# Kernel tuning notes

Measured on AMD Instinct MI355X. Metric: run time of the kernel, lower is better.

## Reference

```python
import jax, jax.numpy as jnp
import numpy as np

STRIDES = (8, 16, 32)
INPUT = (640, 640)
NC = 80           # num_classes
CONF = 0.65       # conf_thr
IOU_THR = 0.65    # nms iou_threshold
K = 1000          # fixed candidate cap for jit-compatible NMS (padded/masked)


def _priors():
    # MlvlPointGenerator(offset=0, with_stride=True): per level, points at
    # (x*stride, y*stride) flattened y-major, format [cx, cy, stride, stride].
    ps = []
    for s in STRIDES:
        H, W = INPUT[0] // s, INPUT[1] // s
        yy, xx = jnp.meshgrid(jnp.arange(H, dtype=jnp.float32),
                              jnp.arange(W, dtype=jnp.float32), indexing='ij')
        cx = (xx * s).ravel()
        cy = (yy * s).ravel()
        st = jnp.full_like(cx, float(s))
        ps.append(jnp.stack([cx, cy, st, st], axis=-1))
    return jnp.concatenate(ps, axis=0)  # [8400, 4]


def _flatten(xs, c):
    # permute(0,2,3,1).reshape(B, -1, c) per level, concat over priors
    return jnp.concatenate(
        [x.transpose(0, 2, 3, 1).reshape(x.shape[0], -1, c) for x in xs], axis=1)


def _decode(priors, bp):
    # bp: [B, N, 4]; priors: [N, 4] (cx, cy, sw, sh)
    xys = bp[..., :2] * priors[:, 2:] + priors[:, :2]
    whs = jnp.exp(bp[..., 2:]) * priors[:, 2:]
    tl = xys - whs * 0.5
    br = xys + whs * 0.5
    return jnp.concatenate([tl, br], axis=-1)  # [B, N, 4] tlbr


def _iou(a, b):
    tl = jnp.maximum(a[:, None, :2], b[None, :, :2])
    br = jnp.minimum(a[:, None, 2:], b[None, :, 2:])
    wh = jnp.clip(br - tl, 0.0)
    inter = wh[..., 0] * wh[..., 1]
    area = lambda x: (x[:, 2] - x[:, 0]) * (x[:, 3] - x[:, 1])
    union = area(a)[:, None] + area(b)[None, :] - inter
    return inter / (union + 1e-6)


def _nms_single(cls_s, obj_s, boxes):
    # cls_s: [N, NC] sigmoid scores; obj_s: [N]; boxes: [N, 4]
    max_s = cls_s.max(axis=-1)
    labels = jnp.argmax(cls_s, axis=-1)
    score = max_s * obj_s
    valid = score >= CONF                       # confidence mask
    sc = jnp.where(valid, score, 0.0)
    top_sc, idx = jax.lax.top_k(sc, K)          # sorted descending -> greedy order
    b = boxes[idx]
    lab = labels[idx]
    v = valid[idx]
    # class-aware (batched) NMS: offset boxes per label so classes never overlap
    max_coord = jnp.max(jnp.abs(b)) + 1.0
    ob = b + (lab.astype(b.dtype) * max_coord)[:, None]
    iou = _iou(ob, ob)                          # [K, K]
    j = jnp.arange(K)
    def body(i, keep):
        sup = (iou[i] > IOU_THR) & (j > i)
        return jnp.where(keep[i] & v[i], keep & (~sup), keep)
    keep = jax.lax.fori_loop(0, K, body, jnp.ones(K, dtype=bool))
    final = keep & v
    dets = jnp.where(final[:, None],
                     jnp.concatenate([b, top_sc[:, None]], axis=-1), 0.0)  # [K, 5]
    labs = jnp.where(final, lab, -1)
    return dets, labs, final


def setup_inputs() -> dict:
    key = jax.random.key(0)
    ks = jax.random.split(key, 9)
    B = 32
    shapes = {
        'cls0': (B, NC, 80, 80), 'cls1': (B, NC, 40, 40), 'cls2': (B, NC, 20, 20),
        'bbox0': (B, 4, 80, 80), 'bbox1': (B, 4, 40, 40), 'bbox2': (B, 4, 20, 20),
        'obj0': (B, 1, 80, 80), 'obj1': (B, 1, 40, 40), 'obj2': (B, 1, 20, 20),
    }
    return {n: jax.random.normal(k, s, dtype=jnp.float32)
            for (n, s), k in zip(shapes.items(), ks)}


def reference(cls0, cls1, cls2, bbox0, bbox1, bbox2, obj0, obj1, obj2):
    priors = _priors()
    cls = jax.nn.sigmoid(_flatten([cls0, cls1, cls2], NC))       # [B, 8400, 80]
    bp = _flatten([bbox0, bbox1, bbox2], 4)                      # [B, 8400, 4]
    obj = jax.nn.sigmoid(_flatten([obj0, obj1, obj2], 1)[..., 0])  # [B, 8400]
    boxes = _decode(priors, bp)                                  # [B, 8400, 4]
    # per-image class-wise batched NMS, padded to K detections
    dets, labels, keep = jax.vmap(_nms_single)(cls, obj, boxes)
    return dets, labels, keep
```

## Files before the change

### kernel.cpp

```cpp
#include <hip/hip_runtime.h>
#include <stdint.h>

#define NPRIOR 8400
#define NB 32
#define NCLS 80
#define KTOP 1000
#define CAP 8400
#define CPAD 16
#define PCH 8
#define CPC 10

typedef unsigned long long u64;

__device__ __forceinline__ float exp_np(float x) {
#pragma clang fp contract(off)
    if (x > 88.72283935546875f) return __builtin_huge_valf();
    if (x < -87.3365478515625f) return 0.0f;
    float q = rintf(x * 1.442695040f);
    float r = fmaf(q, -6.93145752e-1f, x);
    r = fmaf(q, -1.42860677e-6f, r);
    float p = fmaf(1.9875691500e-4f, r, 1.3981999507e-3f);
    p = fmaf(p, r, 8.3334519073e-3f);
    p = fmaf(p, r, 4.1665795894e-2f);
    p = fmaf(p, r, 1.6666665459e-1f);
    p = fmaf(p, r, 5.0000001201e-1f);
    float r2 = r * r;
    p = fmaf(p, r2, r);
    p = p + 1.0f;
    return ldexpf(p, (int)q);
}
__device__ __forceinline__ float sigm_np(float x) {
#pragma clang fp contract(off)
    float t = exp_np(-x);
    return 1.0f / (1.0f + t);
}

__device__ __forceinline__ void level_of(int n, int& W, int& s, int& loc) {
    if (n < 6400)      { W = 80; s = 8;  loc = n; }
    else if (n < 8000) { W = 40; s = 16; loc = n - 6400; }
    else               { W = 20; s = 32; loc = n - 8000; }
}

__device__ float4 decode32(int b, int n,
                           const float* bb0, const float* bb1, const float* bb2) {
#pragma clang fp contract(off)
    int W, s, loc; level_of(n, W, s, loc);
    const float* bb = (s == 8) ? bb0 : (s == 16) ? bb1 : bb2;
    int hw = W * W;
    int y = loc / W, x = loc - y * W;
    const float* bp = bb + (size_t)b * 4 * hw + y * W + x;
    float fs = (float)s;
    float cx = (float)x * fs, cy = (float)y * fs;
    float xc = bp[0] * fs + cx;
    float yc = bp[hw] * fs + cy;
    float wv = exp_np(bp[2 * hw]) * fs;
    float hv = exp_np(bp[3 * hw]) * fs;
    float wv2 = wv * 0.5f, hv2 = hv * 0.5f;
    float4 r;
    r.x = xc - wv2;
    r.y = yc - hv2;
    r.z = xc + wv2;
    r.w = yc + hv2;
    return r;
}

__device__ __forceinline__ u64 packkc(float s, int c) {
    return ((u64)__float_as_uint(s) << 32) | (unsigned)(~(unsigned)c);
}

__global__ void __launch_bounds__(256) score1_k(
    const float* __restrict__ cls0, const float* __restrict__ cls1, const float* __restrict__ cls2,
    u64* __restrict__ part)
{
#pragma clang fp contract(off)
    int b = blockIdx.z, ch = blockIdx.y;
    int g = blockIdx.x * 256 + threadIdx.x;
    if (g >= NPRIOR / 4) return;
    int n0 = g * 4;
    int W, s, loc; level_of(n0, W, s, loc);
    const float* cls = (s == 8) ? cls0 : (s == 16) ? cls1 : cls2;
    int hw = W * W;
    int y = loc / W, x = loc - y * W;
    const float* cp = cls + (size_t)b * NCLS * hw + y * W + x;

    int c0 = ch * CPC;
    float4 v = *(const float4*)(cp + (size_t)c0 * hw);
    u64 k0 = packkc(sigm_np(v.x), c0);
    u64 k1 = packkc(sigm_np(v.y), c0);
    u64 k2 = packkc(sigm_np(v.z), c0);
    u64 k3 = packkc(sigm_np(v.w), c0);
#pragma unroll
    for (int cc = 1; cc < CPC; ++cc) {
        int c = c0 + cc;
        v = *(const float4*)(cp + (size_t)c * hw);
        u64 t;
        t = packkc(sigm_np(v.x), c); if (t > k0) k0 = t;
        t = packkc(sigm_np(v.y), c); if (t > k1) k1 = t;
        t = packkc(sigm_np(v.z), c); if (t > k2) k2 = t;
        t = packkc(sigm_np(v.w), c); if (t > k3) k3 = t;
    }
    u64* p = part + ((size_t)ch * NB + b) * NPRIOR + n0;
    p[0] = k0; p[1] = k1; p[2] = k2; p[3] = k3;
}

__global__ void __launch_bounds__(256) score2_k(
    const float* __restrict__ ob0, const float* __restrict__ ob1, const float* __restrict__ ob2,
    const u64* __restrict__ part,
    float* __restrict__ sc, int* __restrict__ labels,
    u64* __restrict__ keys, int* __restrict__ cnts)
{
#pragma clang fp contract(off)
    int b = blockIdx.y;
    int g = blockIdx.x * 256 + threadIdx.x;
    if (g >= NPRIOR / 4) return;
    int n0 = g * 4;
    int W, s, loc; level_of(n0, W, s, loc);
    const float* ob = (s == 8) ? ob0 : (s == 16) ? ob1 : ob2;
    int hw = W * W;
    int y = loc / W, x = loc - y * W;

    u64 k0 = 0, k1 = 0, k2 = 0, k3 = 0;
#pragma unroll
    for (int ch = 0; ch < PCH; ++ch) {
        const u64* p = part + ((size_t)ch * NB + b) * NPRIOR + n0;
        u64 t0 = p[0], t1 = p[1], t2 = p[2], t3 = p[3];
        if (t0 > k0) k0 = t0;
        if (t1 > k1) k1 = t1;
        if (t2 > k2) k2 = t2;
        if (t3 > k3) k3 = t3;
    }
    float4 tM;
    tM.x = __uint_as_float((unsigned)(k0 >> 32));
    tM.y = __uint_as_float((unsigned)(k1 >> 32));
    tM.z = __uint_as_float((unsigned)(k2 >> 32));
    tM.w = __uint_as_float((unsigned)(k3 >> 32));
    int4 lab;
    lab.x = (int)(~(unsigned)(k0 & 0xffffffffull));
    lab.y = (int)(~(unsigned)(k1 & 0xffffffffull));
    lab.z = (int)(~(unsigned)(k2 & 0xffffffffull));
    lab.w = (int)(~(unsigned)(k3 & 0xffffffffull));

    float4 o = *(const float4*)(ob + (size_t)b * hw + y * W + x);
    float4 sv;
    sv.x = tM.x * sigm_np(o.x);
    sv.y = tM.y * sigm_np(o.y);
    sv.z = tM.z * sigm_np(o.z);
    sv.w = tM.w * sigm_np(o.w);
    float4 scv;
    scv.x = (sv.x >= 0.65f) ? sv.x : 0.0f;
    scv.y = (sv.y >= 0.65f) ? sv.y : 0.0f;
    scv.z = (sv.z >= 0.65f) ? sv.z : 0.0f;
    scv.w = (sv.w >= 0.65f) ? sv.w : 0.0f;
    *(float4*)(sc + (size_t)b * NPRIOR + n0) = scv;
    *(int4*)(labels + (size_t)b * NPRIOR + n0) = lab;

    int lane = threadIdx.x & 63;
#pragma unroll
    for (int e = 0; e < 4; ++e) {
        float se = (e == 0) ? scv.x : (e == 1) ? scv.y : (e == 2) ? scv.z : scv.w;
        bool val = se > 0.0f;
        u64 mb = __ballot(val);
        if (mb) {
            int lead = (int)__builtin_ctzll(mb);
            int base = 0;
            if (lane == lead) base = atomicAdd(&cnts[b * CPAD], (int)__popcll(mb));
            base = __shfl(base, lead);
            if (val) {
                int myoff = (int)__popcll(mb & ((1ull << lane) - 1ull));
                keys[(size_t)b * CAP + base + myoff] =
                    ((u64)__float_as_uint(se) << 32) | (unsigned)(~(unsigned)(n0 + e));
            }
        }
    }
}

__global__ void __launch_bounds__(256) rank_part(
    const u64* __restrict__ keys, const int* __restrict__ cnts,
    int* __restrict__ rankbuf)
{
    int b = blockIdx.y, tid = threadIdx.x;
    int cn = min(cnts[b * CPAD], CAP);
    int nt = (cn + 255) >> 8;
    int ntt = nt * nt;
    const u64* keyimg = keys + (size_t)b * CAP;
    int lane = tid & 63;

    for (int t = blockIdx.x; t < ntt; t += gridDim.x) {
        int it = t / nt, jt = t - it * nt;
        int i = it * 256 + tid;
        u64 ki = (i < cn) ? keyimg[i] : ~0ull;
        int rank = 0;
        int jbase = jt * 256;
        int jend = min(jbase + 256, cn);
        for (int jb = jbase; jb < jend; jb += 64) {
            int j = jb + lane;
            u64 kv = (j < cn) ? keyimg[j] : 0ull;
            unsigned lo = (unsigned)kv, hi = (unsigned)(kv >> 32);
            int lim = jend - jb;
#pragma unroll
            for (int l = 0; l < 64; ++l) {
                unsigned jlo = __builtin_amdgcn_readlane(lo, l);
                unsigned jhi = __builtin_amdgcn_readlane(hi, l);
                u64 kj = ((u64)jhi << 32) | jlo;
                rank += (l < lim && kj > ki) ? 1 : 0;
            }
        }
        if (i < cn && rank > 0) atomicAdd(&rankbuf[(size_t)b * CAP + i], rank);
    }
}

__global__ void __launch_bounds__(256) scatter_k(
    const u64* __restrict__ keys, const int* __restrict__ cnts,
    const int* __restrict__ rankbuf,
    const float* __restrict__ sc, const int* __restrict__ labels,
    const float* __restrict__ bb0, const float* __restrict__ bb1, const float* __restrict__ bb2,
    float4* __restrict__ sel_box, float* __restrict__ sel_score,
    int* __restrict__ sel_label, int* __restrict__ maxbits, u64* __restrict__ vmask)
{
#pragma clang fp contract(off)
    __shared__ float redbuf[256];
    int b = blockIdx.y, chunk = blockIdx.x, tid = threadIdx.x;
    int cn = min(cnts[b * CPAD], CAP);
    int base = chunk * 256;
    if (chunk != 0 && base >= cn) return;

    const u64* keyimg = keys + (size_t)b * CAP;
    const int* labb = labels + (size_t)b * NPRIOR;
    const float* scb = sc + (size_t)b * NPRIOR;

    int i = base + tid;
    float lmax = 0.0f;
    if (i < cn) {
        int rank = rankbuf[(size_t)b * CAP + i];
        if (rank < KTOP) {
            u64 ki = keyimg[i];
            unsigned n = ~(unsigned)(ki & 0xffffffffull);
            float s = __uint_as_float((unsigned)(ki >> 32));
            float4 bx = decode32(b, (int)n, bb0, bb1, bb2);
            sel_box[(size_t)b * 1024 + rank] = bx;
            sel_score[(size_t)b * 1024 + rank] = s;
            sel_label[(size_t)b * 1024 + rank] = labb[n];
            lmax = fmaxf(fmaxf(fabsf(bx.x), fabsf(bx.y)),
                         fmaxf(fabsf(bx.z), fabsf(bx.w)));
        }
    }

    if (chunk == 0) {
        if (cn < KTOP && tid == 0) {
            float lm = 0.0f;
            int r = cn;
            for (int n = 0; n < NPRIOR && r < KTOP; ++n) {
                if (scb[n] == 0.0f) {
                    float4 bx = decode32(b, n, bb0, bb1, bb2);
                    sel_box[(size_t)b * 1024 + r] = bx;
                    sel_score[(size_t)b * 1024 + r] = 0.0f;
                    sel_label[(size_t)b * 1024 + r] = labb[n];
                    lm = fmaxf(lm, fmaxf(fmaxf(fabsf(bx.x), fabsf(bx.y)),
                                         fmaxf(fabsf(bx.z), fabsf(bx.w))));
                    ++r;
                }
            }
            lmax = fmaxf(lmax, lm);
        }
        if (tid < 24) {
            sel_box[(size_t)b * 1024 + 1000 + tid] = make_float4(0.f, 0.f, 0.f, 0.f);
            sel_score[(size_t)b * 1024 + 1000 + tid] = 0.0f;
            sel_label[(size_t)b * 1024 + 1000 + tid] = 0;
        }
        if (tid < 16) {
            int vc = min(cn, KTOP);
            int lo = tid * 64;
            u64 m;
            if (vc >= lo + 64)      m = ~0ull;
            else if (vc <= lo)      m = 0ull;
            else                    m = (1ull << (vc - lo)) - 1ull;
            vmask[b * 16 + tid] = m;
        }
    }

    redbuf[tid] = lmax;
    __syncthreads();
    for (int off = 128; off > 0; off >>= 1) {
        if (tid < off) redbuf[tid] = fmaxf(redbuf[tid], redbuf[tid + off]);
        __syncthreads();
    }
    if (tid == 0) atomicMax(&maxbits[b * CPAD], __float_as_int(redbuf[0]));
}

__global__ void __launch_bounds__(256) build_mask_T(
    const float4* __restrict__ sel_box, const int* __restrict__ sel_label,
    const int* __restrict__ maxbits, u64* __restrict__ Cmask)
{
#pragma clang fp contract(off)
    __shared__ float4 ob[1024];
    __shared__ float ar[1024];
    int b = blockIdx.y, gc = blockIdx.x, tid = threadIdx.x;
    float mc = __int_as_float(maxbits[b * CPAD]) + 1.0f;
    for (int i = tid; i < 1024; i += 256) {
        float4 v = sel_box[(size_t)b * 1024 + i];
        float off = (float)sel_label[(size_t)b * 1024 + i] * mc;
        v.x += off; v.y += off; v.z += off; v.w += off;
        ob[i] = v;
        ar[i] = (v.z - v.x) * (v.w - v.y);
    }
    __syncthreads();
    int wave = tid >> 6, lane = tid & 63;
#pragma unroll
    for (int rgi = 0; rgi < 4; ++rgi) {
        int rg = wave + rgi * 4;
        int row = rg * 64 + lane;
        float4 a = ob[row];
        float aa = ar[row];
        for (int cc = 0; cc < 64; ++cc) {
            int col = gc * 64 + cc;
            bool pred = false;
            if (col > row && row < KTOP && col < KTOP) {
                float4 bb = ob[col];
                float tlx = fmaxf(a.x, bb.x), tly = fmaxf(a.y, bb.y);
                float brx = fminf(a.z, bb.z), bry = fminf(a.w, bb.w);
                float w = fmaxf(brx - tlx, 0.0f), h = fmaxf(bry - tly, 0.0f);
                float inter = w * h;
                float uni = (aa + ar[col]) - inter;
                float iou = inter / (uni + 1e-6f);
                pred = iou > 0.65f;
            }
            u64 bits = __ballot(pred);
            if (lane == 0) Cmask[((size_t)b * 1024 + col) * 16 + rg] = bits;
        }
    }
}

__global__ void __launch_bounds__(64) nms_fixpoint_write(
    const u64* __restrict__ Cmask, const u64* __restrict__ vmask,
    const float4* __restrict__ sel_box, const float* __restrict__ sel_score,
    const int* __restrict__ sel_label, float* __restrict__ out)
{
    int b = blockIdx.x, lane = threadIdx.x;
    const u64* Cimg = Cmask + (size_t)b * 1024 * 16;
    u64 Khist[16];
#pragma unroll
    for (int g = 0; g < 16; ++g) {
        int col = g * 64 + lane;
        const u64* ccol = Cimg + (size_t)col * 16;
        bool supp = false;
#pragma unroll
        for (int gp = 0; gp < g; ++gp)
            supp |= (ccol[gp] & Khist[gp]) != 0ull;
        u64 V = vmask[b * 16 + g] & ~__ballot(supp);
        u64 T = ccol[g];
        u64 K = V;
        for (int it = 0; it < 64; ++it) {
            u64 Knew = V & ~__ballot((T & K) != 0ull);
            if (Knew == K) break;
            K = Knew;
        }
        Khist[g] = K;
    }

    const size_t selo = (size_t)b * 1024;
    float* lab_o = out + (size_t)NB * KTOP * 5;
    float* keep_o = lab_o + (size_t)NB * KTOP;
#pragma unroll
    for (int g = 0; g < 16; ++g) {
        int k = g * 64 + lane;
        if (k >= KTOP) break;
        bool fin = (Khist[g] >> lane) & 1ull;
        float4 bx = sel_box[selo + k];
        float s = sel_score[selo + k];
        int lb = sel_label[selo + k];
        size_t o5 = ((size_t)b * KTOP + k) * 5;
        out[o5 + 0] = fin ? bx.x : 0.0f;
        out[o5 + 1] = fin ? bx.y : 0.0f;
        out[o5 + 2] = fin ? bx.z : 0.0f;
        out[o5 + 3] = fin ? bx.w : 0.0f;
        out[o5 + 4] = fin ? s : 0.0f;
        lab_o[b * KTOP + k] = fin ? (float)lb : -1.0f;
        keep_o[b * KTOP + k] = fin ? 1.0f : 0.0f;
    }
}

extern "C" void kernel_launch(void* const* d_in, const int* in_sizes, int n_in,
                              void* d_out, int out_size, void* d_ws, size_t ws_size,
                              hipStream_t stream) {
    const float* cls0 = (const float*)d_in[0];
    const float* cls1 = (const float*)d_in[1];
    const float* cls2 = (const float*)d_in[2];
    const float* bb0  = (const float*)d_in[3];
    const float* bb1  = (const float*)d_in[4];
    const float* bb2  = (const float*)d_in[5];
    const float* ob0  = (const float*)d_in[6];
    const float* ob1  = (const float*)d_in[7];
    const float* ob2  = (const float*)d_in[8];
    float* out = (float*)d_out;

    char* w = (char*)d_ws;
    size_t used = 0;
    auto alloc = [&](size_t bytes) -> void* {
        void* p = (void*)(w + used);
        used += (bytes + 255) & ~(size_t)255;
        return p;
    };
    float* sc        = (float*)alloc((size_t)NB * NPRIOR * 4);
    int* labels      = (int*)alloc((size_t)NB * NPRIOR * 4);
    u64* keys        = (u64*)alloc((size_t)NB * CAP * 8);
    u64* part        = (u64*)alloc((size_t)PCH * NB * NPRIOR * 8);
    int* zeroed      = (int*)alloc((size_t)(2 * NB * CPAD + NB * CAP) * 4);
    float4* sel_box  = (float4*)alloc((size_t)NB * 1024 * 16);
    float* sel_score = (float*)alloc((size_t)NB * 1024 * 4);
    int* sel_label   = (int*)alloc((size_t)NB * 1024 * 4);
    u64* vmask       = (u64*)alloc((size_t)NB * 16 * 8);
    u64* Cmask       = (u64*)alloc((size_t)NB * 1024 * 16 * 8);

    if (used > ws_size) return;

    int* cnts = zeroed;
    int* maxbits = zeroed + NB * CPAD;
    int* rankbuf = zeroed + 2 * NB * CPAD;
    hipMemsetAsync(zeroed, 0, (size_t)(2 * NB * CPAD + NB * CAP) * 4, stream);

    score1_k<<<dim3((NPRIOR / 4 + 255) / 256, PCH, NB), 256, 0, stream>>>(
        cls0, cls1, cls2, part);
    score2_k<<<dim3((NPRIOR / 4 + 255) / 256, NB), 256, 0, stream>>>(
        ob0, ob1, ob2, part, sc, labels, keys, cnts);
    rank_part<<<dim3(64, NB), 256, 0, stream>>>(keys, cnts, rankbuf);
    scatter_k<<<dim3((CAP + 255) / 256, NB), 256, 0, stream>>>(
        keys, cnts, rankbuf, sc, labels, bb0, bb1, bb2,
        sel_box, sel_score, sel_label, maxbits, vmask);
    build_mask_T<<<dim3(16, NB), 256, 0, stream>>>(sel_box, sel_label, maxbits, Cmask);
    nms_fixpoint_write<<<NB, 64, 0, stream>>>(
        Cmask, vmask, sel_box, sel_score, sel_label, out);
}
```

Measured before the change: 131.8 us.

## Restructure IoU mask build: per-lane column bits, skip lower-triangle tiles, transpose layout

The suppression-mask kernel now gives each lane one column and builds its 64-bit row mask in a register, instead of issuing one ballot and one global store per column. Blocks cover 256x64 tiles, and tiles entirely below the diagonal exit early, which removes redundant IoU work. The Cmask layout becomes [group][col] so both the writes and the fixpoint kernel's reads are coalesced across lanes. The grid grows to 64 blocks per image, and many of those blocks return immediately.

```diff
diff --git a/kernel.cpp b/kernel.cpp
--- a/kernel.cpp
+++ b/kernel.cpp
@@ -292,42 +292,51 @@
     const int* __restrict__ maxbits, u64* __restrict__ Cmask)
 {
 #pragma clang fp contract(off)
-    __shared__ float4 ob[1024];
-    __shared__ float ar[1024];
-    int b = blockIdx.y, gc = blockIdx.x, tid = threadIdx.x;
+    __shared__ float4 obr[256];
+    __shared__ float arr[256];
+    int b = blockIdx.y;
+    int cg = blockIdx.x & 15, rgq = blockIdx.x >> 4;
+    if (rgq * 4 > cg) return;
+    int tid = threadIdx.x, wave = tid >> 6, lane = tid & 63;
     float mc = __int_as_float(maxbits[b * CPAD]) + 1.0f;
-    for (int i = tid; i < 1024; i += 256) {
-        float4 v = sel_box[(size_t)b * 1024 + i];
-        float off = (float)sel_label[(size_t)b * 1024 + i] * mc;
+
+    {
+        int row = rgq * 256 + tid;
+        float4 v = sel_box[(size_t)b * 1024 + row];
+        float off = (float)sel_label[(size_t)b * 1024 + row] * mc;
         v.x += off; v.y += off; v.z += off; v.w += off;
-        ob[i] = v;
-        ar[i] = (v.z - v.x) * (v.w - v.y);
-    }
+        obr[tid] = v;
+        arr[tid] = (v.z - v.x) * (v.w - v.y);
+    }
+    int col = cg * 64 + lane;
+    float4 a = sel_box[(size_t)b * 1024 + col];
+    float offc = (float)sel_label[(size_t)b * 1024 + col] * mc;
+    a.x += offc; a.y += offc; a.z += offc; a.w += offc;
+    float ac = (a.z - a.x) * (a.w - a.y);
     __syncthreads();
-    int wave = tid >> 6, lane = tid & 63;
-#pragma unroll
-    for (int rgi = 0; rgi < 4; ++rgi) {
-        int rg = wave + rgi * 4;
-        int row = rg * 64 + lane;
-        float4 a = ob[row];
-        float aa = ar[row];
-        for (int cc = 0; cc < 64; ++cc) {
-            int col = gc * 64 + cc;
-            bool pred = false;
-            if (col > row && row < KTOP && col < KTOP) {
-                float4 bb = ob[col];
-                float tlx = fmaxf(a.x, bb.x), tly = fmaxf(a.y, bb.y);
-                float brx = fminf(a.z, bb.z), bry = fminf(a.w, bb.w);
-                float w = fmaxf(brx - tlx, 0.0f), h = fmaxf(bry - tly, 0.0f);
-                float inter = w * h;
-                float uni = (aa + ar[col]) - inter;
-                float iou = inter / (uni + 1e-6f);
-                pred = iou > 0.65f;
-            }
-            u64 bits = __ballot(pred);
-            if (lane == 0) Cmask[((size_t)b * 1024 + col) * 16 + rg] = bits;
-        }
-    }
+
+    int rg = rgq * 4 + wave;
+    if (rg > cg) return;
+    int rowbase = rg * 64;
+    u64 bits = 0;
+#pragma unroll 8
+    for (int r = 0; r < 64; ++r) {
+        int row = rowbase + r;
+        float4 rb = obr[wave * 64 + r];
+        float ra = arr[wave * 64 + r];
+        bool pred = false;
+        if (row < col && row < KTOP && col < KTOP) {
+            float tlx = fmaxf(rb.x, a.x), tly = fmaxf(rb.y, a.y);
+            float brx = fminf(rb.z, a.z), bry = fminf(rb.w, a.w);
+            float w = fmaxf(brx - tlx, 0.0f), h = fmaxf(bry - tly, 0.0f);
+            float inter = w * h;
+            float uni = (ra + ac) - inter;
+            float iou = inter / (uni + 1e-6f);
+            pred = iou > 0.65f;
+        }
+        bits |= pred ? (1ull << r) : 0ull;
+    }
+    Cmask[((size_t)b * 16 + rg) * 1024 + col] = bits;
 }
 
 __global__ void __launch_bounds__(64) nms_fixpoint_write(
@@ -336,18 +345,17 @@
     const int* __restrict__ sel_label, float* __restrict__ out)
 {
     int b = blockIdx.x, lane = threadIdx.x;
-    const u64* Cimg = Cmask + (size_t)b * 1024 * 16;
+    const u64* Cimg = Cmask + (size_t)b * 16 * 1024;
     u64 Khist[16];
 #pragma unroll
     for (int g = 0; g < 16; ++g) {
         int col = g * 64 + lane;
-        const u64* ccol = Cimg + (size_t)col * 16;
         bool supp = false;
 #pragma unroll
         for (int gp = 0; gp < g; ++gp)
-            supp |= (ccol[gp] & Khist[gp]) != 0ull;
+            supp |= (Cimg[(size_t)gp * 1024 + col] & Khist[gp]) != 0ull;
         u64 V = vmask[b * 16 + g] & ~__ballot(supp);
-        u64 T = ccol[g];
+        u64 T = Cimg[(size_t)g * 1024 + col];
         u64 K = V;
         for (int it = 0; it < 64; ++it) {
             u64 Knew = V & ~__ballot((T & K) != 0ull);
@@ -409,7 +417,7 @@
     float* sel_score = (float*)alloc((size_t)NB * 1024 * 4);
     int* sel_label   = (int*)alloc((size_t)NB * 1024 * 4);
     u64* vmask       = (u64*)alloc((size_t)NB * 16 * 8);
-    u64* Cmask       = (u64*)alloc((size_t)NB * 1024 * 16 * 8);
+    u64* Cmask       = (u64*)alloc((size_t)NB * 16 * 1024 * 8);
 
     if (used > ws_size) return;
 
@@ -426,7 +434,7 @@
     scatter_k<<<dim3((CAP + 255) / 256, NB), 256, 0, stream>>>(
         keys, cnts, rankbuf, sc, labels, bb0, bb1, bb2,
         sel_box, sel_score, sel_label, maxbits, vmask);
-    build_mask_T<<<dim3(16, NB), 256, 0, stream>>>(sel_box, sel_label, maxbits, Cmask);
+    build_mask_T<<<dim3(64, NB), 256, 0, stream>>>(sel_box, sel_label, maxbits, Cmask);
     nms_fixpoint_write<<<NB, 64, 0, stream>>>(
         Cmask, vmask, sel_box, sel_score, sel_label, out);
 }
```

Measured after the change: 111.3 us. 15.6% less time.
